# Kernel optimization log

Measured on AMD Instinct MI355X. Metric: run time of the kernel, lower is better.

The kernel has to match this reference:

```python
import jax, jax.numpy as jnp
import numpy as np

HEADS = 8
DIM_HEAD = 64
QUERY_DIM = 512
CONTEXT_DIM = 768
INNER_DIM = HEADS * DIM_HEAD  # 512
SCALE = DIM_HEAD ** -0.5


def setup_inputs() -> dict:
    key = jax.random.key(0)
    ks = jax.random.split(key, 7)
    B, N, M = 4, 2048, 1024
    x = jax.random.normal(ks[0], (B, N, QUERY_DIM), dtype=jnp.float32)
    context = jax.random.normal(ks[1], (B, M, CONTEXT_DIM), dtype=jnp.float32)
    # torch Linear weights stored as (out_features, in_features); y = x @ W.T
    Wq = jax.random.normal(ks[2], (INNER_DIM, QUERY_DIM), dtype=jnp.float32) * (QUERY_DIM ** -0.5)
    Wk = jax.random.normal(ks[3], (INNER_DIM, CONTEXT_DIM), dtype=jnp.float32) * (CONTEXT_DIM ** -0.5)
    Wv = jax.random.normal(ks[4], (INNER_DIM, CONTEXT_DIM), dtype=jnp.float32) * (CONTEXT_DIM ** -0.5)
    Wo = jax.random.normal(ks[5], (QUERY_DIM, INNER_DIM), dtype=jnp.float32) * (INNER_DIM ** -0.5)
    bo = jax.random.normal(ks[6], (QUERY_DIM,), dtype=jnp.float32) * 0.01
    return {"x": x, "context": context, "Wq": Wq, "Wk": Wk, "Wv": Wv, "Wo": Wo, "bo": bo}


def reference(x, context, Wq, Wk, Wv, Wo, bo):
    B, N, _ = x.shape
    M = context.shape[1]
    h, d = HEADS, DIM_HEAD
    q = jnp.einsum('bnc,ic->bni', x, Wq)        # [B,N,inner]
    k = jnp.einsum('bmc,ic->bmi', context, Wk)  # [B,M,inner]
    v = jnp.einsum('bmc,ic->bmi', context, Wv)  # [B,M,inner]
    # split heads: b n (h d) -> b h n d
    q = q.reshape(B, N, h, d).transpose(0, 2, 1, 3)
    k = k.reshape(B, M, h, d).transpose(0, 2, 1, 3)
    v = v.reshape(B, M, h, d).transpose(0, 2, 1, 3)
    # fp32 upcast for QK^T (inputs already fp32; kept explicit for fidelity)
    sim = jnp.einsum('bhnd,bhmd->bhnm', q.astype(jnp.float32), k.astype(jnp.float32)) * SCALE
    attn = jax.nn.softmax(sim, axis=-1)
    out = jnp.einsum('bhnm,bhmd->bhnd', attn, v)  # [B,h,N,d]
    out = out.transpose(0, 2, 1, 3).reshape(B, N, h * d)  # b n (h d)
    return jnp.einsum('bni,oi->bno', out, Wo) + bo  # dropout p=0 in eval
```

## Files before the change

### kernel.cpp

```cpp
#include <hip/hip_runtime.h>

using u16 = unsigned short;
typedef __bf16 bf16x8 __attribute__((ext_vector_type(8)));
typedef __bf16 bf16x2 __attribute__((ext_vector_type(2)));
typedef float  f32x4  __attribute__((ext_vector_type(4)));
typedef float  f32x16 __attribute__((ext_vector_type(16)));

#define MFMA16x16x32 __builtin_amdgcn_mfma_f32_16x16x32_bf16
#define MFMA32x32x16 __builtin_amdgcn_mfma_f32_32x32x16_bf16

#if __has_builtin(__builtin_amdgcn_exp2f)
#define EXP2 __builtin_amdgcn_exp2f
#else
#define EXP2 exp2f
#endif

static __device__ __forceinline__ unsigned f2bf_u(float f){
  unsigned x = __builtin_bit_cast(unsigned, f);
  return (x + 0x7fffu + ((x >> 16) & 1u)) >> 16;
}

static __device__ __forceinline__ void gll16(const void* g, void* l){
  __builtin_amdgcn_global_load_lds((const __attribute__((address_space(1))) void*)g,
                                   (__attribute__((address_space(3))) void*)l, 16, 0, 0);
}

static __device__ __forceinline__ f32x16 splat16(float x){
  f32x16 v;
#pragma unroll
  for (int i = 0; i < 16; ++i) v[i] = x;
  return v;
}

__global__ void __launch_bounds__(256) cvt_all(
    const float* __restrict__ x,  u16* __restrict__ xb,
    const float* __restrict__ cx, u16* __restrict__ cxb,
    const float* __restrict__ wq, u16* __restrict__ wqb,
    const float* __restrict__ wk, u16* __restrict__ wkb,
    const float* __restrict__ wv, u16* __restrict__ wvb,
    const float* __restrict__ wo, u16* __restrict__ wob)
{
  const float* in; u16* out; int n4;
  switch (blockIdx.y){
    case 0: in=x;  out=xb;  n4=(4*2048*512)/4; break;
    case 1: in=cx; out=cxb; n4=(4*1024*768)/4; break;
    case 2: in=wq; out=wqb; n4=(512*512)/4;    break;
    case 3: in=wk; out=wkb; n4=(512*768)/4;    break;
    case 4: in=wv; out=wvb; n4=(512*768)/4;    break;
    default:in=wo; out=wob; n4=(512*512)/4;    break;
  }
  int i = blockIdx.x*256 + threadIdx.x;
  const int stride = gridDim.x*256;
  for (; i < n4; i += stride){
    float4 f = ((const float4*)in)[i];
    ushort4 u;
    u.x = (u16)f2bf_u(f.x); u.y = (u16)f2bf_u(f.y);
    u.z = (u16)f2bf_u(f.z); u.w = (u16)f2bf_u(f.w);
    ((ushort4*)out)[i] = u;
  }
}

template<int LDA, int LDB, int KK, int OM>
static __device__ __forceinline__ void gemm_tile64(
    const u16* __restrict__ Ap, const u16* __restrict__ Bp,
    void* __restrict__ Cv, int ldc, int bx, int by,
    const float* __restrict__ bias, float scale,
    u16* __restrict__ sAp, u16* __restrict__ sBp)
{
  const int tid = threadIdx.x;
  const int w = tid >> 6, lane = tid & 63;
  const int wr = w >> 1, wc = w & 1;
  const long tm = (long)bx * 128;
  const long tn = (long)by * 64;

  f32x4 acc[4][2] = {};

  const int srl = lane >> 3, scc = lane & 7;

  auto stage = [&](int kt, int bb){
#pragma unroll
    for (int i = 0; i < 4; ++i){
      const int row = w*32 + i*8 + srl;
      const int sw = scc ^ (row & 7);
      gll16(Ap + (tm + row)*LDA + kt*64 + sw*8, sAp + bb*(128*64) + (w*32 + i*8)*64);
    }
#pragma unroll
    for (int i = 0; i < 2; ++i){
      const int row = w*16 + i*8 + srl;
      const int sw = scc ^ (row & 7);
      gll16(Bp + (tn + row)*LDB + kt*64 + sw*8, sBp + bb*(64*64) + (w*16 + i*8)*64);
    }
  };

  const int fr = lane & 15, fg = lane >> 4;
  constexpr int NK = KK / 64;

  stage(0, 0);
  __syncthreads();
  for (int kt = 0; kt < NK; ++kt){
    if (kt + 1 < NK) stage(kt + 1, (kt + 1) & 1);
    const int bb = kt & 1;
    bf16x8 af[4][2], bfr[2][2];
#pragma unroll
    for (int fm = 0; fm < 4; ++fm){
      const int row = wr*64 + fm*16 + fr;
      const int swz = row & 7;
#pragma unroll
      for (int s = 0; s < 2; ++s)
        af[fm][s] = *(const bf16x8*)&sAp[bb*(128*64) + row*64 + ((s*4 + fg) ^ swz)*8];
    }
#pragma unroll
    for (int fn = 0; fn < 2; ++fn){
      const int row = wc*32 + fn*16 + fr;
      const int swz = row & 7;
#pragma unroll
      for (int s = 0; s < 2; ++s)
        bfr[fn][s] = *(const bf16x8*)&sBp[bb*(64*64) + row*64 + ((s*4 + fg) ^ swz)*8];
    }
#pragma unroll
    for (int s = 0; s < 2; ++s)
#pragma unroll
      for (int fm = 0; fm < 4; ++fm)
#pragma unroll
        for (int fn = 0; fn < 2; ++fn)
          acc[fm][fn] = MFMA16x16x32(af[fm][s], bfr[fn][s], acc[fm][fn], 0, 0, 0);
    __syncthreads();
  }

#pragma unroll
  for (int fm = 0; fm < 4; ++fm){
#pragma unroll
    for (int fn = 0; fn < 2; ++fn){
      const long row0 = tm + wr*64 + fm*16 + fg*4;
      const long col  = tn + wc*32 + fn*16 + fr;
      if (OM == 0){
        u16* C = (u16*)Cv;
#pragma unroll
        for (int rr = 0; rr < 4; ++rr)
          C[(row0 + rr)*ldc + col] = (u16)f2bf_u(acc[fm][fn][rr] * scale);
      } else {
        float* C = (float*)Cv;
        const float bv = bias[col];
#pragma unroll
        for (int rr = 0; rr < 4; ++rr)
          C[(row0 + rr)*ldc + col] = acc[fm][fn][rr] + bv;
      }
    }
  }
}

template<int LDA, int LDB, int KK, int OM>
static __device__ __forceinline__ void gemm_tile128(
    const u16* __restrict__ Ap, const u16* __restrict__ Bp,
    void* __restrict__ Cv, int ldc, int bx, int by,
    const float* __restrict__ bias, float scale,
    u16* __restrict__ sAp, u16* __restrict__ sBp)
{
  const int tid = threadIdx.x;
  const int w = tid >> 6, lane = tid & 63;
  const int wr = w >> 1, wc = w & 1;
  const long tm = (long)bx * 128;
  const long tn = (long)by * 128;

  f32x4 acc[4][4] = {};

  const int srl = lane >> 3, scc = lane & 7;

  auto stage = [&](int kt, int bb){
#pragma unroll
    for (int i = 0; i < 4; ++i){
      const int row = w*32 + i*8 + srl;
      const int sw = scc ^ (row & 7);
      gll16(Ap + (tm + row)*LDA + kt*64 + sw*8, sAp + bb*(128*64) + (w*32 + i*8)*64);
      gll16(Bp + (tn + row)*LDB + kt*64 + sw*8, sBp + bb*(128*64) + (w*32 + i*8)*64);
    }
  };

  const int fr = lane & 15, fg = lane >> 4;
  constexpr int NK = KK / 64;

  stage(0, 0);
  __syncthreads();
  for (int kt = 0; kt < NK; ++kt){
    if (kt + 1 < NK) stage(kt + 1, (kt + 1) & 1);
    const int bb = kt & 1;
    bf16x8 af[4][2], bfr[4][2];
#pragma unroll
    for (int fm = 0; fm < 4; ++fm){
      const int row = wr*64 + fm*16 + fr;
      const int swz = row & 7;
#pragma unroll
      for (int s = 0; s < 2; ++s)
        af[fm][s] = *(const bf16x8*)&sAp[bb*(128*64) + row*64 + ((s*4 + fg) ^ swz)*8];
    }
#pragma unroll
    for (int fn = 0; fn < 4; ++fn){
      const int row = wc*64 + fn*16 + fr;
      const int swz = row & 7;
#pragma unroll
      for (int s = 0; s < 2; ++s)
        bfr[fn][s] = *(const bf16x8*)&sBp[bb*(128*64) + row*64 + ((s*4 + fg) ^ swz)*8];
    }
#pragma unroll
    for (int s = 0; s < 2; ++s)
#pragma unroll
      for (int fm = 0; fm < 4; ++fm)
#pragma unroll
        for (int fn = 0; fn < 4; ++fn)
          acc[fm][fn] = MFMA16x16x32(af[fm][s], bfr[fn][s], acc[fm][fn], 0, 0, 0);
    __syncthreads();
  }

#pragma unroll
  for (int fm = 0; fm < 4; ++fm){
#pragma unroll
    for (int fn = 0; fn < 4; ++fn){
      const long row0 = tm + wr*64 + fm*16 + fg*4;
      const long col  = tn + wc*64 + fn*16 + fr;
      if (OM == 0){
        u16* C = (u16*)Cv;
#pragma unroll
        for (int rr = 0; rr < 4; ++rr)
          C[(row0 + rr)*ldc + col] = (u16)f2bf_u(acc[fm][fn][rr] * scale);
      } else {
        float* C = (float*)Cv;
        const float bv = bias[col];
#pragma unroll
        for (int rr = 0; rr < 4; ++rr)
          C[(row0 + rr)*ldc + col] = acc[fm][fn][rr] + bv;
      }
    }
  }
}

__global__ __launch_bounds__(256, 2) void proj_fused(
    const u16* __restrict__ xb,  const u16* __restrict__ cxb,
    const u16* __restrict__ wqb, const u16* __restrict__ wkb,
    const u16* __restrict__ wvb,
    u16* __restrict__ qb, u16* __restrict__ kb, u16* __restrict__ vtb,
    float qscale)
{
  __shared__ u16 sA[2*128*64];
  __shared__ u16 sB[2*128*64];
  const int bid = blockIdx.x;
  const int lid = (bid & 7)*64 + (bid >> 3);
  if (lid < 256){
    gemm_tile128<512,512,512,0>(xb, wqb, (void*)qb, 512, lid >> 2, lid & 3,
                                nullptr, qscale, sA, sB);
  } else if (lid < 384){
    const int t = lid - 256;
    gemm_tile128<768,768,768,0>(cxb, wkb, (void*)kb, 512, t >> 2, t & 3,
                                nullptr, 1.0f, sA, sB);
  } else {
    const int t = lid - 384, z = t >> 5, r = t & 31;
    gemm_tile128<768,768,768,0>(wvb, cxb + (long)z*1024*768,
                                (void*)(vtb + (long)z*512*1024), 1024,
                                r >> 3, r & 7, nullptr, 1.0f, sA, sB);
  }
}

__global__ __launch_bounds__(256, 3) void gemm_out(
    const u16* __restrict__ ab, const u16* __restrict__ wob,
    float* __restrict__ out, const float* __restrict__ bias)
{
  __shared__ u16 sA[2*128*64];
  __shared__ u16 sB[2*64*64];
  const int bid = blockIdx.x;
  const int lid = (bid & 7)*64 + (bid >> 3);
  gemm_tile64<512,512,512,1>(ab, wob, (void*)out, 512, lid >> 3, lid & 7,
                             bias, 1.0f, sA, sB);
}

__global__ __launch_bounds__(256, 1) void attn_fwd(
    const u16* __restrict__ Q,
    const u16* __restrict__ Kb,
    const u16* __restrict__ Vt,
    u16* __restrict__ O)
{
  const int bid = blockIdx.x;
  const int lid = (bid & 7)*32 + (bid >> 3);
  const int qx = lid & 7, hh = (lid >> 3) & 7, b = lid >> 6;
  const int w = threadIdx.x >> 6, lane = threadIdx.x & 63;
  const int q31 = lane & 31, hi = lane >> 5;
  const int q0 = qx*256 + w*64;

  __shared__ u16 sK[4][64*64];
  __shared__ u16 sV[4][64*64];
  __shared__ float sLs[8*32];

  bf16x8 qf[2][4];
#pragma unroll
  for (int j = 0; j < 2; ++j){
    const u16* qrow = Q + (long)(b*2048 + q0 + j*32 + q31)*512 + hh*64;
#pragma unroll
    for (int ks = 0; ks < 4; ++ks)
      qf[j][ks] = *(const bf16x8*)(qrow + ks*16 + hi*8);
  }

  f32x16 o[2][2] = {{splat16(0.f), splat16(0.f)}, {splat16(0.f), splat16(0.f)}};
  float lsum0 = 0.f, lsum1 = 0.f;

  const int srl = lane >> 3, scc = lane & 7;

  auto stage = [&](int kbv, int bb){
#pragma unroll
    for (int i = 0; i < 2; ++i){
      const int row = w*16 + i*8 + srl;
      const int sw = scc ^ (row & 7);
      gll16(Kb + (long)(b*1024 + kbv*64 + row)*512 + hh*64 + sw*8,
            &sK[bb][(w*16 + i*8)*64]);
      gll16(Vt + (long)(b*512 + hh*64 + row)*1024 + kbv*64 + sw*8,
            &sV[bb][(w*16 + i*8)*64]);
    }
  };

  stage(0, 0);
  stage(1, 1);

  for (int kb = 0; kb < 16; ++kb){
    if (kb + 2 < 16) stage(kb + 2, (kb + 2) & 3);
    if (kb <= 13)      asm volatile("s_waitcnt vmcnt(8)" ::: "memory");
    else if (kb == 14) asm volatile("s_waitcnt vmcnt(4)" ::: "memory");
    else               asm volatile("s_waitcnt vmcnt(0)" ::: "memory");
    __builtin_amdgcn_s_barrier();
    asm volatile("" ::: "memory");
    const u16* sKp = sK[kb & 3];
    const u16* sVp = sV[kb & 3];

#pragma unroll
    for (int mt = 0; mt < 2; ++mt){
      f32x16 s0 = splat16(-16.f), s1 = splat16(-16.f);
      const int row = mt*32 + q31;
      const int swz = row & 7;
      __builtin_amdgcn_s_setprio(1);
#pragma unroll
      for (int ks = 0; ks < 4; ++ks){
        bf16x8 kf = *(const bf16x8*)&sKp[row*64 + ((ks*2 + hi) ^ swz)*8];
        s0 = MFMA32x32x16(kf, qf[0][ks], s0, 0, 0, 0);
        s1 = MFMA32x32x16(kf, qf[1][ks], s1, 0, 0, 0);
      }
      __builtin_amdgcn_s_setprio(0);

      unsigned pk0[8], pk1[8];
#pragma unroll
      for (int r = 0; r < 16; ++r){ s0[r] = EXP2(s0[r]); lsum0 += s0[r]; }
#pragma unroll
      for (int r = 0; r < 16; ++r){ s1[r] = EXP2(s1[r]); lsum1 += s1[r]; }
#pragma unroll
      for (int p2 = 0; p2 < 8; ++p2){
        union { bf16x2 h; unsigned u; } t0, t1;
        t0.h[0] = (__bf16)s0[2*p2]; t0.h[1] = (__bf16)s0[2*p2 + 1]; pk0[p2] = t0.u;
        t1.h[0] = (__bf16)s1[2*p2]; t1.h[1] = (__bf16)s1[2*p2 + 1]; pk1[p2] = t1.u;
      }

#pragma unroll
      for (int sl = 0; sl < 2; ++sl){
        union { unsigned u[4]; bf16x8 v; } pa0, pa1;
        {
          const unsigned ca = pk0[sl*4 + 0], cb = pk0[sl*4 + 1];
          const unsigned cc = pk0[sl*4 + 2], cd = pk0[sl*4 + 3];
          const unsigned ya = hi ? ca : cc;
          const unsigned za = (unsigned)__shfl_xor((int)ya, 32);
          const unsigned yb = hi ? cb : cd;
          const unsigned zb = (unsigned)__shfl_xor((int)yb, 32);
          pa0.u[0] = hi ? za : ca;
          pa0.u[1] = hi ? zb : cb;
          pa0.u[2] = hi ? cc : za;
          pa0.u[3] = hi ? cd : zb;
        }
        {
          const unsigned ca = pk1[sl*4 + 0], cb = pk1[sl*4 + 1];
          const unsigned cc = pk1[sl*4 + 2], cd = pk1[sl*4 + 3];
          const unsigned ya = hi ? ca : cc;
          const unsigned za = (unsigned)__shfl_xor((int)ya, 32);
          const unsigned yb = hi ? cb : cd;
          const unsigned zb = (unsigned)__shfl_xor((int)yb, 32);
          pa1.u[0] = hi ? za : ca;
          pa1.u[1] = hi ? zb : cb;
          pa1.u[2] = hi ? cc : za;
          pa1.u[3] = hi ? cd : zb;
        }
        const int s = mt*2 + sl;
        __builtin_amdgcn_s_setprio(1);
#pragma unroll
        for (int fd = 0; fd < 2; ++fd){
          const int vrow = fd*32 + q31;
          bf16x8 bv = *(const bf16x8*)&sVp[vrow*64 + (((s*2 + hi) ^ (vrow & 7)))*8];
          o[0][fd] = MFMA32x32x16(pa0.v, bv, o[0][fd], 0, 0, 0);
          o[1][fd] = MFMA32x32x16(pa1.v, bv, o[1][fd], 0, 0, 0);
        }
        __builtin_amdgcn_s_setprio(0);
      }
    }
    asm volatile("" ::: "memory");
  }

  lsum0 += __shfl_xor(lsum0, 32);
  lsum1 += __shfl_xor(lsum1, 32);
  sLs[(w*2 + 0)*32 + q31] = lsum0;
  sLs[(w*2 + 1)*32 + q31] = lsum1;
  __syncthreads();

#pragma unroll
  for (int j = 0; j < 2; ++j){
    f32x4 inv[4];
#pragma unroll
    for (int g = 0; g < 4; ++g){
      f32x4 ls = *(const f32x4*)&sLs[(w*2 + j)*32 + 8*g + 4*hi];
#pragma unroll
      for (int e = 0; e < 4; ++e) inv[g][e] = 1.0f / ls[e];
    }
    u16* orow = O + (long)(b*2048 + q0 + j*32)*512 + hh*64;
#pragma unroll
    for (int fd = 0; fd < 2; ++fd){
#pragma unroll
      for (int r = 0; r < 16; ++r){
        const int q = (r & 3) + 8*(r >> 2) + 4*hi;
        const float val = o[j][fd][r] * inv[r >> 2][r & 3];
        orow[(long)q*512 + fd*32 + q31] = (u16)f2bf_u(val);
      }
    }
  }
}

extern "C" void kernel_launch(void* const* d_in, const int* in_sizes, int n_in,
                              void* d_out, int out_size, void* d_ws, size_t ws_size,
                              hipStream_t stream)
{
  (void)in_sizes; (void)n_in; (void)out_size; (void)ws_size;
  const float* x   = (const float*)d_in[0];
  const float* ctx = (const float*)d_in[1];
  const float* Wq  = (const float*)d_in[2];
  const float* Wk  = (const float*)d_in[3];
  const float* Wv  = (const float*)d_in[4];
  const float* Wo  = (const float*)d_in[5];
  const float* bo  = (const float*)d_in[6];
  float* out = (float*)d_out;

  char* ws = (char*)d_ws;
  u16* xb  = (u16*)(ws + 0);
  u16* cxb = (u16*)(ws + 8388608);
  u16* wqb = (u16*)(ws + 14680064);
  u16* wkb = (u16*)(ws + 15204352);
  u16* wvb = (u16*)(ws + 15990784);
  u16* wob = (u16*)(ws + 16777216);
  u16* qb  = (u16*)(ws + 17301504);
  u16* kb  = (u16*)(ws + 25690112);
  u16* vtb = (u16*)(ws + 29884416);
  u16* ab  = (u16*)(ws + 34078720);

  cvt_all<<<dim3(1024, 6, 1), 256, 0, stream>>>(x, xb, ctx, cxb, Wq, wqb,
                                                Wk, wkb, Wv, wvb, Wo, wob);

  proj_fused<<<dim3(512, 1, 1), 256, 0, stream>>>(
      xb, cxb, wqb, wkb, wvb, qb, kb, vtb, 0.18033688011112042f);

  attn_fwd<<<dim3(256, 1, 1), 256, 0, stream>>>(qb, kb, vtb, ab);

  gemm_out<<<dim3(512, 1, 1), 256, 0, stream>>>(ab, wob, out, bo);
}
```

Before: 77.16 us.

## Split attention KV loop across two wave groups with LDS reduction

The attention kernel now runs 512 threads per block. Two groups of four waves each process alternating KV tiles for the same query rows, so each wave does half the KV iterations. The partial outputs and row sums are then combined through LDS, reusing the K buffer as scratch, before normalization and store. This is meant to raise per-CU parallelism and latency hiding, since the grid is only 256 blocks, at the cost of doubled LDS buffers, an extra reduction phase with more barriers, and register pressure under the new launch bounds.

```diff
diff --git a/kernel.cpp b/kernel.cpp
--- a/kernel.cpp
+++ b/kernel.cpp
@@ -271,7 +271,7 @@
                              bias, 1.0f, sA, sB);
 }
 
-__global__ __launch_bounds__(256, 1) void attn_fwd(
+__global__ __launch_bounds__(512, 2) void attn_fwd(
     const u16* __restrict__ Q,
     const u16* __restrict__ Kb,
     const u16* __restrict__ Vt,
@@ -282,11 +282,13 @@
   const int qx = lid & 7, hh = (lid >> 3) & 7, b = lid >> 6;
   const int w = threadIdx.x >> 6, lane = threadIdx.x & 63;
   const int q31 = lane & 31, hi = lane >> 5;
-  const int q0 = qx*256 + w*64;
-
-  __shared__ u16 sK[4][64*64];
-  __shared__ u16 sV[4][64*64];
-  __shared__ float sLs[8*32];
+  const int w4 = w & 3, kvg = w >> 2;
+  const int q0 = qx*256 + w4*64;
+
+  __shared__ u16 sK[8][64*64];
+  __shared__ u16 sV[8][64*64];
+  __shared__ float sLsP[16*32];
+  __shared__ float sLsT[8*32];
 
   bf16x8 qf[2][4];
 #pragma unroll
@@ -302,30 +304,34 @@
 
   const int srl = lane >> 3, scc = lane & 7;
 
-  auto stage = [&](int kbv, int bb){
+  auto stagePair = [&](int u){
+    const int tv = 2*u + kvg;
+    const int sl = tv & 7;
 #pragma unroll
     for (int i = 0; i < 2; ++i){
-      const int row = w*16 + i*8 + srl;
+      const int row = w4*16 + i*8 + srl;
       const int sw = scc ^ (row & 7);
-      gll16(Kb + (long)(b*1024 + kbv*64 + row)*512 + hh*64 + sw*8,
-            &sK[bb][(w*16 + i*8)*64]);
-      gll16(Vt + (long)(b*512 + hh*64 + row)*1024 + kbv*64 + sw*8,
-            &sV[bb][(w*16 + i*8)*64]);
+      gll16(Kb + (long)(b*1024 + tv*64 + row)*512 + hh*64 + sw*8,
+            &sK[sl][(w4*16 + i*8)*64]);
+      gll16(Vt + (long)(b*512 + hh*64 + row)*1024 + tv*64 + sw*8,
+            &sV[sl][(w4*16 + i*8)*64]);
     }
   };
 
-  stage(0, 0);
-  stage(1, 1);
-
-  for (int kb = 0; kb < 16; ++kb){
-    if (kb + 2 < 16) stage(kb + 2, (kb + 2) & 3);
-    if (kb <= 13)      asm volatile("s_waitcnt vmcnt(8)" ::: "memory");
-    else if (kb == 14) asm volatile("s_waitcnt vmcnt(4)" ::: "memory");
-    else               asm volatile("s_waitcnt vmcnt(0)" ::: "memory");
+  stagePair(0);
+  stagePair(1);
+
+  for (int t = 0; t < 8; ++t){
+    if (t + 2 < 8) stagePair(t + 2);
+    if (t <= 5)      asm volatile("s_waitcnt vmcnt(8)" ::: "memory");
+    else if (t == 6) asm volatile("s_waitcnt vmcnt(4)" ::: "memory");
+    else             asm volatile("s_waitcnt vmcnt(0)" ::: "memory");
     __builtin_amdgcn_s_barrier();
     asm volatile("" ::: "memory");
-    const u16* sKp = sK[kb & 3];
-    const u16* sVp = sV[kb & 3];
+    const int tv = 2*t + kvg;
+    const int sl = tv & 7;
+    const u16* sKp = sK[sl];
+    const u16* sVp = sV[sl];
 
 #pragma unroll
     for (int mt = 0; mt < 2; ++mt){
@@ -354,11 +360,11 @@
       }
 
 #pragma unroll
-      for (int sl = 0; sl < 2; ++sl){
+      for (int sl2 = 0; sl2 < 2; ++sl2){
         union { unsigned u[4]; bf16x8 v; } pa0, pa1;
         {
-          const unsigned ca = pk0[sl*4 + 0], cb = pk0[sl*4 + 1];
-          const unsigned cc = pk0[sl*4 + 2], cd = pk0[sl*4 + 3];
+          const unsigned ca = pk0[sl2*4 + 0], cb = pk0[sl2*4 + 1];
+          const unsigned cc = pk0[sl2*4 + 2], cd = pk0[sl2*4 + 3];
           const unsigned ya = hi ? ca : cc;
           const unsigned za = (unsigned)__shfl_xor((int)ya, 32);
           const unsigned yb = hi ? cb : cd;
@@ -369,8 +375,8 @@
           pa0.u[3] = hi ? cd : zb;
         }
         {
-          const unsigned ca = pk1[sl*4 + 0], cb = pk1[sl*4 + 1];
-          const unsigned cc = pk1[sl*4 + 2], cd = pk1[sl*4 + 3];
+          const unsigned ca = pk1[sl2*4 + 0], cb = pk1[sl2*4 + 1];
+          const unsigned cc = pk1[sl2*4 + 2], cd = pk1[sl2*4 + 3];
           const unsigned ya = hi ? ca : cc;
           const unsigned za = (unsigned)__shfl_xor((int)ya, 32);
           const unsigned yb = hi ? cb : cd;
@@ -380,7 +386,7 @@
           pa1.u[2] = hi ? cc : za;
           pa1.u[3] = hi ? cd : zb;
         }
-        const int s = mt*2 + sl;
+        const int s = mt*2 + sl2;
         __builtin_amdgcn_s_setprio(1);
 #pragma unroll
         for (int fd = 0; fd < 2; ++fd){
@@ -397,27 +403,69 @@
 
   lsum0 += __shfl_xor(lsum0, 32);
   lsum1 += __shfl_xor(lsum1, 32);
-  sLs[(w*2 + 0)*32 + q31] = lsum0;
-  sLs[(w*2 + 1)*32 + q31] = lsum1;
+  sLsP[(w*2 + 0)*32 + q31] = lsum0;
+  sLsP[(w*2 + 1)*32 + q31] = lsum1;
   __syncthreads();
 
-#pragma unroll
-  for (int j = 0; j < 2; ++j){
-    f32x4 inv[4];
-#pragma unroll
-    for (int g = 0; g < 4; ++g){
-      f32x4 ls = *(const f32x4*)&sLs[(w*2 + j)*32 + 8*g + 4*hi];
-#pragma unroll
-      for (int e = 0; e < 4; ++e) inv[g][e] = 1.0f / ls[e];
-    }
-    u16* orow = O + (long)(b*2048 + q0 + j*32)*512 + hh*64;
-#pragma unroll
-    for (int fd = 0; fd < 2; ++fd){
-#pragma unroll
-      for (int r = 0; r < 16; ++r){
-        const int q = (r & 3) + 8*(r >> 2) + 4*hi;
-        const float val = o[j][fd][r] * inv[r >> 2][r & 3];
-        orow[(long)q*512 + fd*32 + q31] = (u16)f2bf_u(val);
+  float* sO = (float*)&sK[0][0];
+  if (w >= 4){
+#pragma unroll
+    for (int j = 0; j < 2; ++j){
+#pragma unroll
+      for (int fd = 0; fd < 2; ++fd){
+        float* p = sO + ((((w - 4)*2 + j)*2 + fd)*64*20) + lane*20;
+#pragma unroll
+        for (int k = 0; k < 4; ++k){
+          f32x4 t4;
+#pragma unroll
+          for (int e = 0; e < 4; ++e) t4[e] = o[j][fd][4*k + e];
+          *(f32x4*)(p + 4*k) = t4;
+        }
+      }
+    }
+  }
+  __syncthreads();
+
+  if (w < 4){
+#pragma unroll
+    for (int j = 0; j < 2; ++j){
+#pragma unroll
+      for (int fd = 0; fd < 2; ++fd){
+        const float* p = sO + (((w*2 + j)*2 + fd)*64*20) + lane*20;
+#pragma unroll
+        for (int k = 0; k < 4; ++k){
+          f32x4 t4 = *(const f32x4*)(p + 4*k);
+#pragma unroll
+          for (int e = 0; e < 4; ++e) o[j][fd][4*k + e] += t4[e];
+        }
+      }
+    }
+    const float lt0 = lsum0 + sLsP[((w + 4)*2 + 0)*32 + q31];
+    const float lt1 = lsum1 + sLsP[((w + 4)*2 + 1)*32 + q31];
+    sLsT[(w*2 + 0)*32 + q31] = lt0;
+    sLsT[(w*2 + 1)*32 + q31] = lt1;
+  }
+  __syncthreads();
+
+  if (w < 4){
+#pragma unroll
+    for (int j = 0; j < 2; ++j){
+      f32x4 inv[4];
+#pragma unroll
+      for (int g = 0; g < 4; ++g){
+        f32x4 ls = *(const f32x4*)&sLsT[(w*2 + j)*32 + 8*g + 4*hi];
+#pragma unroll
+        for (int e = 0; e < 4; ++e) inv[g][e] = 1.0f / ls[e];
+      }
+      u16* orow = O + (long)(b*2048 + q0 + j*32)*512 + hh*64;
+#pragma unroll
+      for (int fd = 0; fd < 2; ++fd){
+#pragma unroll
+        for (int r = 0; r < 16; ++r){
+          const int q = (r & 3) + 8*(r >> 2) + 4*hi;
+          const float val = o[j][fd][r] * inv[r >> 2][r & 3];
+          orow[(long)q*512 + fd*32 + q31] = (u16)f2bf_u(val);
+        }
       }
     }
   }
@@ -455,7 +503,7 @@
   proj_fused<<<dim3(512, 1, 1), 256, 0, stream>>>(
       xb, cxb, wqb, wkb, wvb, qb, kb, vtb, 0.18033688011112042f);
 
-  attn_fwd<<<dim3(256, 1, 1), 256, 0, stream>>>(qb, kb, vtb, ab);
+  attn_fwd<<<dim3(256, 1, 1), 512, 0, stream>>>(qb, kb, vtb, ab);
 
   gemm_out<<<dim3(512, 1, 1), 256, 0, stream>>>(ab, wob, out, bo);
 }
```

Result: faster. 67.19 us (-12.9%).
